# Performance work log

Hardware: AMD Instinct MI355X
Metric: run time of the kernel (lower is better)

The kernel has to match this reference:

```python
import jax, jax.numpy as jnp
import numpy as np

N = 50000   # nodes
E = 1600000 # edges
G = 512     # graphs in batch
IN_DIM, EMBED, H, D = 64, 128, 4, 32
D1, D2, D3 = 128, 64, 16
NEG_SLOPE = 0.2  # DGL GATConv default


def setup_inputs() -> dict:
    key = jax.random.key(0)
    ks = jax.random.split(key, 16)
    def glorot(k, shape):
        fan = shape[0] + shape[-1]
        return jax.random.normal(k, shape, jnp.float32) * jnp.sqrt(2.0 / fan)
    return {
        "feature": jax.random.normal(ks[0], (N, IN_DIM), jnp.float32),
        "src": jax.random.randint(ks[1], (E,), 0, N, jnp.int32),
        "dst": jax.random.randint(ks[2], (E,), 0, N, jnp.int32),
        "graph_ids": jnp.sort(jax.random.randint(ks[3], (N,), 0, G, jnp.int32)),
        "W0": glorot(ks[4], (IN_DIM, EMBED)), "b0": jnp.zeros((EMBED,), jnp.float32),
        "Wfc": glorot(ks[5], (EMBED, H * D)),
        "attn_l": glorot(ks[6], (H, D)), "attn_r": glorot(ks[7], (H, D)),
        "gat_bias": jnp.zeros((H * D,), jnp.float32),
        "W1": glorot(ks[8], (H * D, D1)), "b1": jnp.zeros((D1,), jnp.float32),
        "W2": glorot(ks[9], (D1, D2)), "b2": jnp.zeros((D2,), jnp.float32),
        "W3": glorot(ks[10], (D2, D3)), "b3": jnp.zeros((D3,), jnp.float32),
    }


def reference(feature, src, dst, graph_ids, W0, b0, Wfc, attn_l, attn_r,
              gat_bias, W1, b1, W2, b2, W3, b3):
    # initial dense embed
    h = feature @ W0 + b0                                   # [N, EMBED]
    # GATConv
    feat = (h @ Wfc).reshape(N, H, D)                       # [N,H,D]
    el = jnp.einsum('nhd,hd->nh', feat, attn_l)             # [N,H]
    er = jnp.einsum('nhd,hd->nh', feat, attn_r)
    e = jax.nn.leaky_relu(el[src] + er[dst], NEG_SLOPE)     # [E,H]
    # segment softmax over incoming edges of each dst node
    m = jax.ops.segment_max(e, dst, num_segments=N)         # [N,H]
    ex = jnp.exp(e - m[dst])                                # [E,H]
    denom = jax.ops.segment_sum(ex, dst, num_segments=N)    # [N,H]
    a = ex / denom[dst]                                     # [E,H]
    msg = a[:, :, None] * feat[src]                         # [E,H,D]
    rst = jax.ops.segment_sum(msg, dst, num_segments=N)     # [N,H,D]
    rst = rst + gat_bias.reshape(1, H, D)
    hn = rst.reshape(N, H * D)
    # AvgPooling per graph
    sums = jax.ops.segment_sum(hn, graph_ids, num_segments=G)           # [G,H*D]
    cnts = jax.ops.segment_sum(jnp.ones((N,), hn.dtype), graph_ids, num_segments=G)
    hg = sums / jnp.maximum(cnts, 1.0)[:, None]
    # dense head
    out = jax.nn.elu(hg)
    out = jax.nn.elu(out @ W1 + b1)
    out = jax.nn.elu(out @ W2 + b2)
    out = out @ W3 + b3                                     # [G, D3]
    atten = a[:, :, None]                                   # [E,H,1] like DGL
    return out, atten
```

## Files before the change

kernel.cpp:

```cpp
#include <hip/hip_runtime.h>
#include <hip/hip_fp16.h>
#include <math.h>

#define N_NODES 50000
#define E_EDGES 1600000
#define G_GRAPHS 512
#define IN_DIM 64
#define EMBED 128
#define HD 128
#define NHEAD 4
#define D1 128
#define D2 64
#define D3 16
#define NEG_SLOPE 0.2f
#define NB ((N_NODES + 127) >> 7)
#define PT_TILE 4096
#define PT_BLOCKS ((E_EDGES + PT_TILE - 1) / PT_TILE)
#define FB_CAP 8192

typedef float vfloat4 __attribute__((ext_vector_type(4)));
typedef float vfloat2 __attribute__((ext_vector_type(2)));
typedef unsigned short ushort_t;

static __device__ __forceinline__ float leaky(float x) { return x > 0.f ? x : NEG_SLOPE * x; }
static __device__ __forceinline__ float compf(float4 v, int i) {
    return i == 0 ? v.x : (i == 1 ? v.y : (i == 2 ? v.z : v.w));
}

__global__ void __launch_bounds__(256) k0hg(const int* __restrict__ dst, int* __restrict__ ghist,
                                            const float* __restrict__ W0, const float* __restrict__ b0,
                                            const float* __restrict__ Wfc, float* __restrict__ Wc,
                                            float* __restrict__ bc) {
    __shared__ int lh[NB];
    const int t = threadIdx.x;
    if (blockIdx.x < PT_BLOCKS) {
        for (int i = t; i < NB; i += 256) lh[i] = 0;
        __syncthreads();
        const long e0 = (long)blockIdx.x * PT_TILE;
#pragma unroll
        for (int k = 0; k < PT_TILE / 256; ++k) {
            long e = e0 + t + k * 256;
            if (e < E_EDGES) atomicAdd(&lh[dst[e] >> 7], 1);
        }
        __syncthreads();
        for (int i = t; i < NB; i += 256) {
            int v = lh[i];
            if (v) atomicAdd(&ghist[i], v);
        }
    } else {
        int tid = (int)(blockIdx.x - PT_BLOCKS) * 256 + t;
        if (tid < IN_DIM * HD) {
            int i = tid >> 7, j = tid & 127;
            float acc = 0.f;
            for (int k = 0; k < EMBED; ++k) acc += W0[i * EMBED + k] * Wfc[k * HD + j];
            Wc[tid] = acc;
        } else if (tid < IN_DIM * HD + HD) {
            int j = tid - IN_DIM * HD;
            float acc = 0.f;
            for (int k = 0; k < EMBED; ++k) acc += b0[k] * Wfc[k * HD + j];
            bc[j] = acc;
        }
    }
}

__global__ void __launch_bounds__(256) k1_gemm(const float* __restrict__ A,
                                               const float* __restrict__ W,
                                               const float* __restrict__ b,
                                               const float* __restrict__ attn_l,
                                               const float* __restrict__ attn_r,
                                               unsigned char* __restrict__ feat,
                                               float* __restrict__ el,
                                               float* __restrict__ er) {
    __shared__ float Ws[IN_DIM * HD];
    __shared__ float As[32][65];
    __shared__ float fs[32][132];
    const int t = threadIdx.x;
    const int c = t & 127, rr = t >> 7;
    const int row0 = blockIdx.x * 32;
    for (int i = t; i < IN_DIM * HD; i += 256) Ws[i] = W[i];
    for (int i = t; i < 32 * IN_DIM; i += 256) {
        int r = i >> 6, k = i & 63;
        int gr = row0 + r;
        As[r][k] = (gr < N_NODES) ? A[(size_t)gr * IN_DIM + k] : 0.f;
    }
    __syncthreads();
    float acc[16];
#pragma unroll
    for (int i = 0; i < 16; ++i) acc[i] = 0.f;
    for (int k = 0; k < IN_DIM; ++k) {
        float w = Ws[k * HD + c];
#pragma unroll
        for (int i = 0; i < 16; ++i) acc[i] += As[rr * 16 + i][k] * w;
    }
    const float bb = b[c];
#pragma unroll
    for (int i = 0; i < 16; ++i) fs[rr * 16 + i][c] = acc[i] + bb;
    __syncthreads();
    {
        const int row = t >> 3, s = t & 7;
        const int gr = row0 + row;
        if (gr < N_NODES) {
            unsigned int w[4];
#pragma unroll
            for (int k = 0; k < 4; ++k) {
                unsigned int ww = __builtin_amdgcn_cvt_pk_fp8_f32(
                    fs[row][s * 16 + 4 * k], fs[row][s * 16 + 4 * k + 1], 0, false);
                ww = __builtin_amdgcn_cvt_pk_fp8_f32(
                    fs[row][s * 16 + 4 * k + 2], fs[row][s * 16 + 4 * k + 3], ww, true);
                w[k] = ww;
            }
            *(uint4*)(feat + (size_t)gr * HD + s * 16) = make_uint4(w[0], w[1], w[2], w[3]);
        }
    }
    {
        const int r = t >> 3, q = t & 7, c0 = q * 16, h = q >> 1;
        float pl = 0.f, pr = 0.f;
#pragma unroll
        for (int k = 0; k < 16; ++k) {
            float f = fs[r][c0 + k];
            pl += f * attn_l[c0 + k];
            pr += f * attn_r[c0 + k];
        }
        pl += __shfl_xor(pl, 1);
        pr += __shfl_xor(pr, 1);
        if ((t & 1) == 0) {
            int n = row0 + r;
            if (n < N_NODES) {
                el[n * 4 + h] = pl;
                er[n * 4 + h] = pr;
            }
        }
    }
}

__global__ void __launch_bounds__(64) sc_scan(const int* __restrict__ ghist,
                                              int* __restrict__ coarse_start,
                                              int* __restrict__ cursorp) {
    const int lane = threadIdx.x;
    int run = 0;
    for (int c = 0; c < (NB + 63) / 64; ++c) {
        int i = c * 64 + lane;
        int v = (i < NB) ? ghist[i] : 0;
        int incl = v;
#pragma unroll
        for (int off = 1; off < 64; off <<= 1) {
            int o = __shfl_up(incl, off, 64);
            if (lane >= off) incl += o;
        }
        if (i < NB) {
            coarse_start[i] = run + incl - v;
            cursorp[i] = run + incl - v;
        }
        run += __shfl(incl, 63, 64);
    }
    if (lane == 0) coarse_start[NB] = E_EDGES;
}

__global__ void __launch_bounds__(256) pt_partition(const int* __restrict__ src,
                                                    const int* __restrict__ dst,
                                                    int* __restrict__ cursorp,
                                                    unsigned int* __restrict__ part) {
    __shared__ int hist[4][NB];
    __shared__ int tot[NB], offs[NB], base_s[NB];
    __shared__ int lcur[4][NB];
    __shared__ unsigned int stage[PT_TILE];
    const int t = threadIdx.x, lane = t & 63, wid = t >> 6;
    const long e0 = (long)blockIdx.x * PT_TILE;
    const int cnt = (int)min((long)PT_TILE, (long)E_EDGES - e0);
    for (int i = t; i < NB; i += 256) {
        hist[0][i] = 0; hist[1][i] = 0; hist[2][i] = 0; hist[3][i] = 0;
    }
    __syncthreads();
    unsigned int v[PT_TILE / 256];
#pragma unroll
    for (int k = 0; k < PT_TILE / 256; ++k) {
        int i = t + k * 256;
        if (i < cnt) {
            int d = dst[e0 + i];
            v[k] = ((unsigned int)d << 16) | (unsigned int)src[e0 + i];
            atomicAdd(&hist[wid][d >> 7], 1);
        } else v[k] = 0xFFFFFFFFu;
    }
    __syncthreads();
    for (int i = t; i < NB; i += 256) {
        int h0 = hist[0][i], h1 = hist[1][i], h2 = hist[2][i], h3 = hist[3][i];
        hist[0][i] = 0; hist[1][i] = h0; hist[2][i] = h0 + h1; hist[3][i] = h0 + h1 + h2;
        tot[i] = h0 + h1 + h2 + h3;
    }
    __syncthreads();
    if (wid == 0) {
        int run = 0;
        for (int c = 0; c < (NB + 63) / 64; ++c) {
            int i = c * 64 + lane;
            int vv = (i < NB) ? tot[i] : 0;
            int incl = vv;
#pragma unroll
            for (int off = 1; off < 64; off <<= 1) {
                int o = __shfl_up(incl, off, 64);
                if (lane >= off) incl += o;
            }
            if (i < NB) offs[i] = run + incl - vv;
            run += __shfl(incl, 63, 64);
        }
    }
    __syncthreads();
    for (int i = t; i < NB; i += 256) {
        int tt = tot[i];
        base_s[i] = tt ? atomicAdd(&cursorp[i], tt) : 0;
        int ob = offs[i];
        lcur[0][i] = ob + hist[0][i];
        lcur[1][i] = ob + hist[1][i];
        lcur[2][i] = ob + hist[2][i];
        lcur[3][i] = ob + hist[3][i];
    }
    __syncthreads();
#pragma unroll
    for (int k = 0; k < PT_TILE / 256; ++k) {
        if (v[k] != 0xFFFFFFFFu) {
            int b = v[k] >> 23;
            int pos = atomicAdd(&lcur[wid][b], 1);
            stage[pos] = v[k];
        }
    }
    __syncthreads();
    for (int i = t; i < cnt; i += 256) {
        unsigned int p = stage[i];
        int b = p >> 23;
        part[base_s[b] + (i - offs[b])] = p & 0x7FFFFFu;
    }
}

__global__ void __launch_bounds__(256) fb_fill(const unsigned int* __restrict__ part,
                                               const int* __restrict__ coarse_start,
                                               int* __restrict__ rowstart,
                                               ushort_t* __restrict__ csr_src) {
    const int b = blockIdx.x, t = threadIdx.x, lane = t & 63, wid = t >> 6;
    const int s0 = coarse_start[b], s1 = coarse_start[b + 1];
    const int cnt = s1 - s0;
    __shared__ int degl[4][128], totl[128], offl[128], curl[4][128];
    __shared__ ushort_t lsrc[FB_CAP];
    if (t < 128) { degl[0][t] = 0; degl[1][t] = 0; degl[2][t] = 0; degl[3][t] = 0; }
    __syncthreads();
    for (int i = t; i < cnt; i += 256) {
        unsigned int p = part[s0 + i];
        atomicAdd(&degl[wid][p >> 16], 1);
    }
    __syncthreads();
    if (t < 128) {
        int d0 = degl[0][t], d1 = degl[1][t], d2 = degl[2][t], d3 = degl[3][t];
        degl[0][t] = 0; degl[1][t] = d0; degl[2][t] = d0 + d1; degl[3][t] = d0 + d1 + d2;
        totl[t] = d0 + d1 + d2 + d3;
    }
    __syncthreads();
    if (wid == 0) {
        int run = 0;
        for (int c = 0; c < 2; ++c) {
            int i = c * 64 + lane;
            int vv = totl[i];
            int incl = vv;
#pragma unroll
            for (int off = 1; off < 64; off <<= 1) {
                int o = __shfl_up(incl, off, 64);
                if (lane >= off) incl += o;
            }
            offl[i] = run + incl - vv;
            run += __shfl(incl, 63, 64);
        }
    }
    __syncthreads();
    if (t < 128) {
        int ob = offl[t];
        curl[0][t] = ob + degl[0][t];
        curl[1][t] = ob + degl[1][t];
        curl[2][t] = ob + degl[2][t];
        curl[3][t] = ob + degl[3][t];
        int node = (b << 7) + t;
        if (node < N_NODES) rowstart[node] = s0 + ob;
    }
    if (b == 0 && t == 0) rowstart[N_NODES] = E_EDGES;
    __syncthreads();
    if (cnt <= FB_CAP) {
        for (int i = t; i < cnt; i += 256) {
            unsigned int p = part[s0 + i];
            int pos = atomicAdd(&curl[wid][p >> 16], 1);
            lsrc[pos] = (ushort_t)(p & 0xFFFFu);
        }
        __syncthreads();
        for (int i = t; i < cnt; i += 256) csr_src[s0 + i] = lsrc[i];
    } else {
        for (int i = t; i < cnt; i += 256) {
            unsigned int p = part[s0 + i];
            int pos = atomicAdd(&curl[wid][p >> 16], 1);
            csr_src[s0 + pos] = (ushort_t)(p & 0xFFFFu);
        }
    }
}

__global__ void __launch_bounds__(256) k6_aggregate(
    const ushort_t* __restrict__ csr_src, const int* __restrict__ rowstart,
    const float* __restrict__ el, const float* __restrict__ er,
    const unsigned char* __restrict__ feat, const float* __restrict__ gat_bias,
    float* __restrict__ er_rd, float* __restrict__ hn) {
    __shared__ float s_av[4][64][4];
    __shared__ int s_src[4][64];
    const int wid = threadIdx.x >> 6;
    const int lane = threadIdx.x & 63;
    const int n = blockIdx.x * 4 + wid;
    if (n >= N_NODES) return;
    const int start = rowstart[n];
    const int end = rowstart[n + 1];
    const int deg = end - start;
    const float4 er4 = *(const float4*)(er + n * 4);

    int esrc = 0;
    float4 ex = make_float4(0.f, 0.f, 0.f, 0.f);
    const bool valid = lane < deg;
    if (valid) {
        esrc = csr_src[start + lane];
        const float4 elv = *(const float4*)(el + esrc * 4);
        ex.x = __expf(leaky(elv.x + er4.x));
        ex.y = __expf(leaky(elv.y + er4.y));
        ex.z = __expf(leaky(elv.z + er4.z));
        ex.w = __expf(leaky(elv.w + er4.w));
    }
    float4 sm = ex;
    for (int e = start + lane + 64; e < end; e += 64) {
        int s = csr_src[e];
        const float4 elv = *(const float4*)(el + s * 4);
        sm.x += __expf(leaky(elv.x + er4.x));
        sm.y += __expf(leaky(elv.y + er4.y));
        sm.z += __expf(leaky(elv.z + er4.z));
        sm.w += __expf(leaky(elv.w + er4.w));
    }
#pragma unroll
    for (int off = 32; off; off >>= 1) {
        sm.x += __shfl_xor(sm.x, off);
        sm.y += __shfl_xor(sm.y, off);
        sm.z += __shfl_xor(sm.z, off);
        sm.w += __shfl_xor(sm.w, off);
    }
    float4 rd;
    rd.x = sm.x > 0.f ? 1.f / sm.x : 0.f;
    rd.y = sm.y > 0.f ? 1.f / sm.y : 0.f;
    rd.z = sm.z > 0.f ? 1.f / sm.z : 0.f;
    rd.w = sm.w > 0.f ? 1.f / sm.w : 0.f;
    if (lane == 0) {
        *(float4*)(er_rd + (size_t)n * 8) = er4;
        *(float4*)(er_rd + (size_t)n * 8 + 4) = rd;
    }
    vfloat4 av4;
    av4.x = ex.x * rd.x;
    av4.y = ex.y * rd.y;
    av4.z = ex.z * rd.z;
    av4.w = ex.w * rd.w;
    s_src[wid][lane] = valid ? esrc : 0;
    *(vfloat4*)(&s_av[wid][lane][0]) = av4;

    const int g4 = lane >> 4, gl = lane & 15;
    const int h = gl >> 2;
    float4 a0 = make_float4(0.f, 0.f, 0.f, 0.f);
    float4 a1 = make_float4(0.f, 0.f, 0.f, 0.f);

    if (deg <= 64) {
        const int iters = (deg + 3) >> 2;
        int idx = g4;
        for (int it = 0; it < iters; ++it, idx += 4) {
            const float av = s_av[wid][idx][h];
            const unsigned int cs = (unsigned int)s_src[wid][idx];
            const uint2 w = *(const uint2*)(feat + (size_t)cs * HD + gl * 8);
            const vfloat2 p0 = __builtin_amdgcn_cvt_pk_f32_fp8(w.x, false);
            const vfloat2 p1 = __builtin_amdgcn_cvt_pk_f32_fp8(w.x, true);
            const vfloat2 p2 = __builtin_amdgcn_cvt_pk_f32_fp8(w.y, false);
            const vfloat2 p3 = __builtin_amdgcn_cvt_pk_f32_fp8(w.y, true);
            a0.x += av * p0.x; a0.y += av * p0.y;
            a0.z += av * p1.x; a0.w += av * p1.y;
            a1.x += av * p2.x; a1.y += av * p2.y;
            a1.z += av * p3.x; a1.w += av * p3.y;
        }
    } else {
        const float rh = compf(rd, h);
        const float erh = compf(er4, h);
        for (int e = start + g4; e < end; e += 4) {
            const unsigned int s = csr_src[e];
            const float av = __expf(leaky(el[s * 4 + h] + erh)) * rh;
            const uint2 w = *(const uint2*)(feat + (size_t)s * HD + gl * 8);
            const vfloat2 p0 = __builtin_amdgcn_cvt_pk_f32_fp8(w.x, false);
            const vfloat2 p1 = __builtin_amdgcn_cvt_pk_f32_fp8(w.x, true);
            const vfloat2 p2 = __builtin_amdgcn_cvt_pk_f32_fp8(w.y, false);
            const vfloat2 p3 = __builtin_amdgcn_cvt_pk_f32_fp8(w.y, true);
            a0.x += av * p0.x; a0.y += av * p0.y;
            a0.z += av * p1.x; a0.w += av * p1.y;
            a1.x += av * p2.x; a1.y += av * p2.y;
            a1.z += av * p3.x; a1.w += av * p3.y;
        }
    }
#pragma unroll
    for (int off = 16; off <= 32; off <<= 1) {
        a0.x += __shfl_xor(a0.x, off);
        a0.y += __shfl_xor(a0.y, off);
        a0.z += __shfl_xor(a0.z, off);
        a0.w += __shfl_xor(a0.w, off);
        a1.x += __shfl_xor(a1.x, off);
        a1.y += __shfl_xor(a1.y, off);
        a1.z += __shfl_xor(a1.z, off);
        a1.w += __shfl_xor(a1.w, off);
    }
    if (lane < 16) {
        const float4 b0 = ((const float4*)gat_bias)[gl * 2];
        const float4 b1 = ((const float4*)gat_bias)[gl * 2 + 1];
        float4* hp = (float4*)(hn + (size_t)n * HD + gl * 8);
        hp[0] = make_float4(a0.x + b0.x, a0.y + b0.y, a0.z + b0.z, a0.w + b0.w);
        hp[1] = make_float4(a1.x + b1.x, a1.y + b1.y, a1.z + b1.z, a1.w + b1.w);
    }
}

__global__ void __launch_bounds__(256) k6b_attn(
    const int* __restrict__ src, const int* __restrict__ dst,
    const float* __restrict__ el, const float* __restrict__ er_rd,
    float* __restrict__ a_out) {
    int e = blockIdx.x * 256 + threadIdx.x;
    if (e >= E_EDGES) return;
    const int s = src[e], d = dst[e];
    const float4 el4 = *(const float4*)(el + s * 4);
    const float4 er4 = *(const float4*)(er_rd + (size_t)d * 8);
    const float4 r4 = *(const float4*)(er_rd + (size_t)d * 8 + 4);
    vfloat4 a;
    a.x = __expf(leaky(el4.x + er4.x)) * r4.x;
    a.y = __expf(leaky(el4.y + er4.y)) * r4.y;
    a.z = __expf(leaky(el4.z + er4.z)) * r4.z;
    a.w = __expf(leaky(el4.w + er4.w)) * r4.w;
    __builtin_nontemporal_store(a, (vfloat4*)a_out + e);
}

__global__ void __launch_bounds__(512) k7_pool_mlp(
    const float* __restrict__ hn, const int* __restrict__ graph_ids,
    const float* __restrict__ W1, const float* __restrict__ b1,
    const float* __restrict__ W2, const float* __restrict__ b2,
    const float* __restrict__ W3, const float* __restrict__ b3,
    float* __restrict__ out) {
    const int g = blockIdx.x, t = threadIdx.x;
    const int tt = t & 127, part = t >> 7;
    __shared__ int bounds[2];
    __shared__ double pool[4][128];
    __shared__ double x[128], y[128];
    if (t < 2) {
        const int target = g + t;
        int lo = 0, hi = N_NODES;
        while (lo < hi) {
            int mid = (lo + hi) >> 1;
            if (graph_ids[mid] < target) lo = mid + 1; else hi = mid;
        }
        bounds[t] = lo;
    }
    __syncthreads();
    const int lo = bounds[0], hi = bounds[1];
    double s = 0.0;
    for (int n = lo + part; n < hi; n += 4) s += (double)hn[(size_t)n * HD + tt];
    pool[part][tt] = s;
    __syncthreads();
    if (t < 128) {
        const double cnt = (double)(hi - lo);
        const double sum = pool[0][t] + pool[1][t] + pool[2][t] + pool[3][t];
        const double v = sum / fmax(cnt, 1.0);
        x[t] = v > 0.0 ? v : expm1(v);
    }
    __syncthreads();
    if (t < 128) {
        double acc = (double)b1[t];
        for (int k = 0; k < HD; ++k) acc += x[k] * (double)W1[k * D1 + t];
        y[t] = acc > 0.0 ? acc : expm1(acc);
    }
    __syncthreads();
    if (t < D2) {
        double a2 = (double)b2[t];
        for (int k = 0; k < D1; ++k) a2 += y[k] * (double)W2[k * D2 + t];
        x[t] = a2 > 0.0 ? a2 : expm1(a2);
    }
    __syncthreads();
    if (t < D3) {
        double a3 = (double)b3[t];
        for (int k = 0; k < D2; ++k) a3 += x[k] * (double)W3[k * D3 + t];
        out[g * D3 + t] = (float)a3;
    }
}

extern "C" void kernel_launch(void* const* d_in, const int* in_sizes, int n_in,
                              void* d_out, int out_size, void* d_ws, size_t ws_size,
                              hipStream_t stream) {
    const float* feature = (const float*)d_in[0];
    const int* src = (const int*)d_in[1];
    const int* dst = (const int*)d_in[2];
    const int* graph_ids = (const int*)d_in[3];
    const float* W0 = (const float*)d_in[4];
    const float* b0 = (const float*)d_in[5];
    const float* Wfc = (const float*)d_in[6];
    const float* attn_l = (const float*)d_in[7];
    const float* attn_r = (const float*)d_in[8];
    const float* gat_bias = (const float*)d_in[9];
    const float* W1 = (const float*)d_in[10];
    const float* b1 = (const float*)d_in[11];
    const float* W2 = (const float*)d_in[12];
    const float* b2 = (const float*)d_in[13];
    const float* W3 = (const float*)d_in[14];
    const float* b3 = (const float*)d_in[15];

    char* ws = (char*)d_ws;
    size_t off = 0;
    auto carve = [&](size_t bytes) -> void* {
        void* p = ws + off;
        off += (bytes + 255) & ~(size_t)255;
        return p;
    };
    int* ghist = (int*)carve((size_t)NB * 4);
    const size_t zero_span = off;
    int* coarse_start = (int*)carve((size_t)(NB + 1) * 4);
    int* cursorp = (int*)carve((size_t)NB * 4);
    float* Wc = (float*)carve((size_t)IN_DIM * HD * 4);
    float* bc = (float*)carve((size_t)HD * 4);
    unsigned char* feat = (unsigned char*)carve((size_t)N_NODES * HD);
    float* el = (float*)carve((size_t)N_NODES * 4 * 4);
    float* er = (float*)carve((size_t)N_NODES * 4 * 4);
    float* er_rd = (float*)carve((size_t)N_NODES * 8 * 4);
    int* rowstart = (int*)carve((size_t)(N_NODES + 1) * 4);
    unsigned int* part = (unsigned int*)carve((size_t)E_EDGES * 4);
    ushort_t* csr_src = (ushort_t*)carve((size_t)E_EDGES * 2);

    float* out = (float*)d_out;
    float* hn = out + G_GRAPHS * D3;
    float* a_out = hn;

    (void)hipMemsetAsync(d_ws, 0, zero_span, stream);
    k0hg<<<PT_BLOCKS + 33, 256, 0, stream>>>(dst, ghist, W0, b0, Wfc, Wc, bc);
    k1_gemm<<<(N_NODES + 31) / 32, 256, 0, stream>>>(feature, Wc, bc, attn_l, attn_r,
                                                     feat, el, er);
    sc_scan<<<1, 64, 0, stream>>>(ghist, coarse_start, cursorp);
    pt_partition<<<PT_BLOCKS, 256, 0, stream>>>(src, dst, cursorp, part);
    fb_fill<<<NB, 256, 0, stream>>>(part, coarse_start, rowstart, csr_src);
    k6_aggregate<<<(N_NODES + 3) / 4, 256, 0, stream>>>(csr_src, rowstart, el, er, feat,
                                                        gat_bias, er_rd, hn);
    k7_pool_mlp<<<G_GRAPHS, 512, 0, stream>>>(hn, graph_ids, W1, b1, W2, b2, W3, b3, out);
    k6b_attn<<<(E_EDGES + 255) / 256, 256, 0, stream>>>(src, dst, el, er_rd, a_out);
}
```

Before: 266.0 us.

## Register-tile k1_gemm with 8x4 per-thread blocks and vectorized LDS loads

Rewrites the node-embedding GEMM so each thread computes an 8-row by 4-column register tile over 64 rows per block, using float4 global and LDS loads. The fp8 feature pack and the el/er attention dot products are computed directly from registers, with shuffle reductions, so the staging shared-memory tile and its extra barrier go away. This raises arithmetic intensity per LDS read and halves the block count. In exchange it uses more registers per thread, and the feature stores become 4-byte writes instead of 16-byte writes.

```diff
diff --git a/kernel.cpp b/kernel.cpp
--- a/kernel.cpp
+++ b/kernel.cpp
@@ -71,63 +71,96 @@
                                                unsigned char* __restrict__ feat,
                                                float* __restrict__ el,
                                                float* __restrict__ er) {
-    __shared__ float Ws[IN_DIM * HD];
-    __shared__ float As[32][65];
-    __shared__ float fs[32][132];
+    __shared__ __align__(16) float Ws[IN_DIM * HD];
+    __shared__ __align__(16) float As[64][68];
     const int t = threadIdx.x;
-    const int c = t & 127, rr = t >> 7;
-    const int row0 = blockIdx.x * 32;
-    for (int i = t; i < IN_DIM * HD; i += 256) Ws[i] = W[i];
-    for (int i = t; i < 32 * IN_DIM; i += 256) {
-        int r = i >> 6, k = i & 63;
-        int gr = row0 + r;
-        As[r][k] = (gr < N_NODES) ? A[(size_t)gr * IN_DIM + k] : 0.f;
-    }
-    __syncthreads();
-    float acc[16];
-#pragma unroll
-    for (int i = 0; i < 16; ++i) acc[i] = 0.f;
-    for (int k = 0; k < IN_DIM; ++k) {
-        float w = Ws[k * HD + c];
-#pragma unroll
-        for (int i = 0; i < 16; ++i) acc[i] += As[rr * 16 + i][k] * w;
-    }
-    const float bb = b[c];
-#pragma unroll
-    for (int i = 0; i < 16; ++i) fs[rr * 16 + i][c] = acc[i] + bb;
-    __syncthreads();
+    const int cc = t & 31;
+    const int rt = t >> 5;
+    const int c0 = cc * 4;
+    const int r0 = rt * 8;
+    const int row0 = blockIdx.x * 64;
+
     {
-        const int row = t >> 3, s = t & 7;
-        const int gr = row0 + row;
+        const float4* Wg = (const float4*)W;
+        float4* Wl = (float4*)Ws;
+#pragma unroll
+        for (int j = 0; j < (IN_DIM * HD / 4) / 256; ++j) Wl[t + j * 256] = Wg[t + j * 256];
+    }
+#pragma unroll
+    for (int j = 0; j < 4; ++j) {
+        int i2 = t + j * 256;
+        int row = i2 >> 4, kq = i2 & 15;
+        int gr = row0 + row;
+        float4 v = (gr < N_NODES) ? *(const float4*)(A + (size_t)gr * IN_DIM + kq * 4)
+                                  : make_float4(0.f, 0.f, 0.f, 0.f);
+        *(float4*)&As[row][kq * 4] = v;
+    }
+    __syncthreads();
+
+    float acc[8][4];
+#pragma unroll
+    for (int i = 0; i < 8; ++i)
+#pragma unroll
+        for (int j = 0; j < 4; ++j) acc[i][j] = 0.f;
+
+    for (int k4 = 0; k4 < IN_DIM / 4; ++k4) {
+        vfloat4 w0 = *(const vfloat4*)&Ws[(k4 * 4 + 0) * HD + c0];
+        vfloat4 w1 = *(const vfloat4*)&Ws[(k4 * 4 + 1) * HD + c0];
+        vfloat4 w2 = *(const vfloat4*)&Ws[(k4 * 4 + 2) * HD + c0];
+        vfloat4 w3 = *(const vfloat4*)&Ws[(k4 * 4 + 3) * HD + c0];
+#pragma unroll
+        for (int i = 0; i < 8; ++i) {
+            vfloat4 a = *(const vfloat4*)&As[r0 + i][k4 * 4];
+#pragma unroll
+            for (int j = 0; j < 4; ++j)
+                acc[i][j] += a.x * w0[j] + a.y * w1[j] + a.z * w2[j] + a.w * w3[j];
+        }
+    }
+
+    {
+        vfloat4 bcv = *(const vfloat4*)(b + c0);
+#pragma unroll
+        for (int i = 0; i < 8; ++i)
+#pragma unroll
+            for (int j = 0; j < 4; ++j) acc[i][j] += bcv[j];
+    }
+
+#pragma unroll
+    for (int i = 0; i < 8; ++i) {
+        int gr = row0 + r0 + i;
         if (gr < N_NODES) {
-            unsigned int w[4];
-#pragma unroll
-            for (int k = 0; k < 4; ++k) {
-                unsigned int ww = __builtin_amdgcn_cvt_pk_fp8_f32(
-                    fs[row][s * 16 + 4 * k], fs[row][s * 16 + 4 * k + 1], 0, false);
-                ww = __builtin_amdgcn_cvt_pk_fp8_f32(
-                    fs[row][s * 16 + 4 * k + 2], fs[row][s * 16 + 4 * k + 3], ww, true);
-                w[k] = ww;
+            unsigned int ww = __builtin_amdgcn_cvt_pk_fp8_f32(acc[i][0], acc[i][1], 0, false);
+            ww = __builtin_amdgcn_cvt_pk_fp8_f32(acc[i][2], acc[i][3], ww, true);
+            *(unsigned int*)(feat + (size_t)gr * HD + c0) = ww;
+        }
+    }
+
+    {
+        vfloat4 al = *(const vfloat4*)(attn_l + c0);
+        vfloat4 ar = *(const vfloat4*)(attn_r + c0);
+        float pl[8], pr[8];
+#pragma unroll
+        for (int i = 0; i < 8; ++i) {
+            pl[i] = acc[i][0] * al[0] + acc[i][1] * al[1] + acc[i][2] * al[2] + acc[i][3] * al[3];
+            pr[i] = acc[i][0] * ar[0] + acc[i][1] * ar[1] + acc[i][2] * ar[2] + acc[i][3] * ar[3];
+        }
+#pragma unroll
+        for (int off = 1; off <= 4; off <<= 1) {
+#pragma unroll
+            for (int i = 0; i < 8; ++i) {
+                pl[i] += __shfl_xor(pl[i], off);
+                pr[i] += __shfl_xor(pr[i], off);
             }
-            *(uint4*)(feat + (size_t)gr * HD + s * 16) = make_uint4(w[0], w[1], w[2], w[3]);
-        }
-    }
-    {
-        const int r = t >> 3, q = t & 7, c0 = q * 16, h = q >> 1;
-        float pl = 0.f, pr = 0.f;
-#pragma unroll
-        for (int k = 0; k < 16; ++k) {
-            float f = fs[r][c0 + k];
-            pl += f * attn_l[c0 + k];
-            pr += f * attn_r[c0 + k];
-        }
-        pl += __shfl_xor(pl, 1);
-        pr += __shfl_xor(pr, 1);
-        if ((t & 1) == 0) {
-            int n = row0 + r;
-            if (n < N_NODES) {
-                el[n * 4 + h] = pl;
-                er[n * 4 + h] = pr;
+        }
+        if ((cc & 7) == 0) {
+            const int h = cc >> 3;
+#pragma unroll
+            for (int i = 0; i < 8; ++i) {
+                int gr = row0 + r0 + i;
+                if (gr < N_NODES) {
+                    el[gr * 4 + h] = pl[i];
+                    er[gr * 4 + h] = pr[i];
+                }
             }
         }
     }
@@ -531,7 +564,7 @@
 
     (void)hipMemsetAsync(d_ws, 0, zero_span, stream);
     k0hg<<<PT_BLOCKS + 33, 256, 0, stream>>>(dst, ghist, W0, b0, Wfc, Wc, bc);
-    k1_gemm<<<(N_NODES + 31) / 32, 256, 0, stream>>>(feature, Wc, bc, attn_l, attn_r,
+    k1_gemm<<<(N_NODES + 63) / 64, 256, 0, stream>>>(feature, Wc, bc, attn_l, attn_r,
                                                      feat, el, er);
     sc_scan<<<1, 64, 0, stream>>>(ghist, coarse_start, cursorp);
     pt_partition<<<PT_BLOCKS, 256, 0, stream>>>(src, dst, cursorp, part);
```

Measured after the change: 243.7 us. -8.4%, faster.
